# Kernel tuning notes

Measured on AMD Instinct MI355X. Metric: run time of the kernel, lower is better.

The kernel has to match this reference:

```python
import jax, jax.numpy as jnp
import numpy as np

D_MODEL = 1024
N_HEADS = 16
D_HEAD = D_MODEL // N_HEADS
D_FF = 4096
B, T = 2, 2048


def setup_inputs() -> dict:
    key = jax.random.key(0)
    ks = jax.random.split(key, 7)
    s = lambda fan_in: 1.0 / np.sqrt(fan_in)
    return {
        "x": jax.random.normal(ks[0], (B, T, D_MODEL), dtype=jnp.float32),
        "ln1_g": jnp.ones((D_MODEL,), jnp.float32),
        "ln1_b": jnp.zeros((D_MODEL,), jnp.float32),
        "w_qkv": jax.random.normal(ks[1], (D_MODEL, 3 * D_MODEL), jnp.float32) * s(D_MODEL),
        "w_proj": jax.random.normal(ks[2], (D_MODEL, D_MODEL), jnp.float32) * s(D_MODEL),
        "ln2_g": jnp.ones((D_MODEL,), jnp.float32),
        "ln2_b": jnp.zeros((D_MODEL,), jnp.float32),
        "w_fc1": jax.random.normal(ks[3], (D_MODEL, D_FF), jnp.float32) * s(D_MODEL),
        "w_fc2": jax.random.normal(ks[4], (D_FF, D_MODEL), jnp.float32) * s(D_FF),
    }


def _layernorm(x, g, b, eps=1e-5):
    mu = jnp.mean(x, axis=-1, keepdims=True)
    var = jnp.var(x, axis=-1, keepdims=True)
    return (x - mu) * jax.lax.rsqrt(var + eps) * g + b


def _attn(x, w_qkv, w_proj):
    Bx, Tx, d = x.shape
    qkv = x @ w_qkv  # [B,T,3d]
    q, k, v = jnp.split(qkv, 3, axis=-1)
    split = lambda t: t.reshape(Bx, Tx, N_HEADS, D_HEAD).transpose(0, 2, 1, 3)
    q, k, v = split(q), split(k), split(v)
    scores = jnp.einsum("bhqd,bhkd->bhqk", q, k) / np.sqrt(D_HEAD).astype(np.float32)
    mask = jnp.tril(jnp.ones((Tx, Tx), dtype=bool))
    scores = jnp.where(mask, scores, -jnp.inf)
    attn = jax.nn.softmax(scores, axis=-1)
    out = jnp.einsum("bhqk,bhkd->bhqd", attn, v)
    out = out.transpose(0, 2, 1, 3).reshape(Bx, Tx, d)
    return out @ w_proj


def reference(x, ln1_g, ln1_b, w_qkv, w_proj, ln2_g, ln2_b, w_fc1, w_fc2):
    x = x + _attn(_layernorm(x, ln1_g, ln1_b), w_qkv, w_proj)
    h = jax.nn.gelu(_layernorm(x, ln2_g, ln2_b) @ w_fc1, approximate=False)
    return x + h @ w_fc2
```

## Files before the change

kernel.cpp:

```cpp
#include <hip/hip_runtime.h>
#include <math.h>

using short8 = __attribute__((ext_vector_type(8))) short;
using f32x4  = __attribute__((ext_vector_type(4))) float;
typedef unsigned short ushort;

__device__ inline ushort f2bf(float f) {
    union { float f; unsigned int i; } v; v.f = f;
    unsigned int x = v.i;
    return (ushort)((x + 0x7FFFu + ((x >> 16) & 1u)) >> 16);
}
__device__ inline void st_out(float* p, float v) { *p = v; }
__device__ inline void st_out(ushort* p, float v) { *p = f2bf(v); }

__device__ inline void gl_lds16(const ushort* g, ushort* l) {
    __builtin_amdgcn_global_load_lds((const __attribute__((address_space(1))) unsigned int*)g,
                                     (__attribute__((address_space(3))) unsigned int*)l, 16, 0, 0);
}
#define MFMA __builtin_amdgcn_mfma_f32_16x16x32_bf16

__global__ __launch_bounds__(256) void ln_kernel(const float* __restrict__ x,
                                                 const float* __restrict__ g,
                                                 const float* __restrict__ b,
                                                 ushort* __restrict__ y) {
    int row = blockIdx.x;
    const float* xr = x + (size_t)row * 1024;
    int t = threadIdx.x;
    float v[4];
    float s = 0.f, s2 = 0.f;
#pragma unroll
    for (int i = 0; i < 4; i++) {
        v[i] = xr[t + i * 256];
        s += v[i]; s2 += v[i] * v[i];
    }
#pragma unroll
    for (int off = 1; off < 64; off <<= 1) {
        s += __shfl_xor(s, off); s2 += __shfl_xor(s2, off);
    }
    __shared__ float ps[8];
    int w = t >> 6;
    if ((t & 63) == 0) { ps[w] = s; ps[4 + w] = s2; }
    __syncthreads();
    s  = ps[0] + ps[1] + ps[2] + ps[3];
    s2 = ps[4] + ps[5] + ps[6] + ps[7];
    float mu   = s * (1.0f / 1024.0f);
    float var  = s2 * (1.0f / 1024.0f) - mu * mu;
    float rinv = rsqrtf(var + 1e-5f);
    ushort* yr = y + (size_t)row * 1024;
#pragma unroll
    for (int i = 0; i < 4; i++) {
        int c = t + i * 256;
        yr[c] = f2bf((v[i] - mu) * rinv * g[c] + b[c]);
    }
}

__global__ __launch_bounds__(256) void wt_kernel(const float* __restrict__ s,
                                                 ushort* __restrict__ d, int K, int N) {
    __shared__ float tile[32][33];
    int n0 = blockIdx.x * 32, k0 = blockIdx.y * 32;
    int tx = threadIdx.x & 31, ty = threadIdx.x >> 5;
#pragma unroll
    for (int i = 0; i < 4; i++)
        tile[ty + i * 8][tx] = s[(size_t)(k0 + ty + i * 8) * N + n0 + tx];
    __syncthreads();
#pragma unroll
    for (int i = 0; i < 4; i++)
        d[(size_t)(n0 + ty + i * 8) * K + k0 + tx] = f2bf(tile[tx][ty + i * 8]);
}

template <int EPI, typename CT>
__global__ __launch_bounds__(256) void gemm_kernel(const ushort* __restrict__ A,
                                                   const ushort* __restrict__ Bt,
                                                   CT* __restrict__ C,
                                                   const float* __restrict__ R,
                                                   ushort* __restrict__ VT,
                                                   int M, int N, int K) {
    __shared__ alignas(16) ushort As[128 * 32];
    __shared__ alignas(16) ushort Bs[128 * 32];
    int t = threadIdx.x, lane = t & 63, w = t >> 6;
    int bm = blockIdx.y * 128, bn = blockIdx.x * 128;
    int wm = (w >> 1) * 64, wn = (w & 1) * 64;
    f32x4 acc[4][4] = {};
    int srow = lane >> 2;
    int schunk = (lane & 3) ^ ((lane >> 3) & 3);
    int rs = lane & 15, qd = lane >> 4;

    for (int k0 = 0; k0 < K; k0 += 32) {
        __syncthreads();
#pragma unroll
        for (int i = 0; i < 2; i++) {
            int idx = w * 2 + i;
            gl_lds16(A  + (size_t)(bm + idx * 16 + srow) * K + k0 + schunk * 8, &As[idx * 512]);
            gl_lds16(Bt + (size_t)(bn + idx * 16 + srow) * K + k0 + schunk * 8, &Bs[idx * 512]);
        }
        __syncthreads();
        short8 af[4], bf[4];
#pragma unroll
        for (int i = 0; i < 4; i++) {
            int ml = wm + i * 16 + rs;
            af[i] = *(const short8*)&As[ml * 32 + ((qd ^ ((ml >> 1) & 3)) * 8)];
            int nl = wn + i * 16 + rs;
            bf[i] = *(const short8*)&Bs[nl * 32 + ((qd ^ ((nl >> 1) & 3)) * 8)];
        }
#pragma unroll
        for (int mi = 0; mi < 4; mi++)
#pragma unroll
            for (int ni = 0; ni < 4; ni++)
                acc[mi][ni] = MFMA(af[mi], bf[ni], acc[mi][ni], 0, 0, 0);
    }
#pragma unroll
    for (int mi = 0; mi < 4; mi++)
#pragma unroll
        for (int ni = 0; ni < 4; ni++) {
            int row = bm + wm + mi * 16 + qd * 4;
            int col = bn + wn + ni * 16 + rs;
            if (EPI == 3) {
                if (col < 2048) {
#pragma unroll
                    for (int r = 0; r < 4; r++)
                        ((ushort*)C)[(size_t)(row + r) * 2048 + col] = f2bf(acc[mi][ni][r]);
                } else {
                    int rel = col - 2048, hh = rel >> 6, dd = rel & 63;
                    ushort tmp[4];
#pragma unroll
                    for (int r = 0; r < 4; r++) tmp[r] = f2bf(acc[mi][ni][r]);
                    size_t base = ((size_t)((row >> 11) * 16 + hh) * 64 + dd) * 2048 + (row & 2047);
                    *(uint2*)&VT[base] = *(uint2*)tmp;
                }
            } else {
#pragma unroll
                for (int r = 0; r < 4; r++) {
                    float v = acc[mi][ni][r];
                    size_t idx = (size_t)(row + r) * N + col;
                    if (EPI == 1) v += R[idx];
                    if (EPI == 2) v = 0.5f * v * (1.0f + erff(v * 0.70710678118f));
                    st_out(&C[idx], v);
                }
            }
        }
}

template <int EPI, typename CT>
__global__ __launch_bounds__(256) void gemm_n64_kernel(const ushort* __restrict__ A,
                                                       const ushort* __restrict__ Bt,
                                                       CT* __restrict__ C,
                                                       const float* __restrict__ R,
                                                       int M, int N, int K) {
    __shared__ alignas(16) ushort As[128 * 32];
    __shared__ alignas(16) ushort Bs[64 * 32];
    int t = threadIdx.x, lane = t & 63, w = t >> 6;
    int bm = blockIdx.y * 128, bn = blockIdx.x * 64;
    int wm = (w >> 1) * 64, wn = (w & 1) * 32;
    f32x4 acc[4][2] = {};
    int srow = lane >> 2;
    int schunk = (lane & 3) ^ ((lane >> 3) & 3);
    int rs = lane & 15, qd = lane >> 4;

    for (int k0 = 0; k0 < K; k0 += 32) {
        __syncthreads();
#pragma unroll
        for (int i = 0; i < 2; i++) {
            int idx = w * 2 + i;
            gl_lds16(A + (size_t)(bm + idx * 16 + srow) * K + k0 + schunk * 8, &As[idx * 512]);
        }
        gl_lds16(Bt + (size_t)(bn + w * 16 + srow) * K + k0 + schunk * 8, &Bs[w * 512]);
        __syncthreads();
        short8 af[4], bf[2];
#pragma unroll
        for (int i = 0; i < 4; i++) {
            int ml = wm + i * 16 + rs;
            af[i] = *(const short8*)&As[ml * 32 + ((qd ^ ((ml >> 1) & 3)) * 8)];
        }
#pragma unroll
        for (int j = 0; j < 2; j++) {
            int nl = wn + j * 16 + rs;
            bf[j] = *(const short8*)&Bs[nl * 32 + ((qd ^ ((nl >> 1) & 3)) * 8)];
        }
#pragma unroll
        for (int mi = 0; mi < 4; mi++)
#pragma unroll
            for (int ni = 0; ni < 2; ni++)
                acc[mi][ni] = MFMA(af[mi], bf[ni], acc[mi][ni], 0, 0, 0);
    }
#pragma unroll
    for (int mi = 0; mi < 4; mi++)
#pragma unroll
        for (int ni = 0; ni < 2; ni++) {
            int row = bm + wm + mi * 16 + qd * 4;
            int col = bn + wn + ni * 16 + rs;
#pragma unroll
            for (int r = 0; r < 4; r++) {
                float v = acc[mi][ni][r];
                size_t idx = (size_t)(row + r) * N + col;
                if (EPI == 1) v += R[idx];
                if (EPI == 2) v = 0.5f * v * (1.0f + erff(v * 0.70710678118f));
                st_out(&C[idx], v);
            }
        }
}

__global__ __launch_bounds__(256) void attn_kernel(const ushort* __restrict__ qk,
                                                   const ushort* __restrict__ vT,
                                                   ushort* __restrict__ outp) {
    __shared__ alignas(16) ushort Ks[128 * 64];
    __shared__ alignas(16) ushort VTs[64 * 128];
    __shared__ alignas(16) ushort Ps[4 * 16 * 136];
    int t = threadIdx.x, lane = t & 63, w = t >> 6;
    int q0 = (int)(gridDim.x - 1 - blockIdx.x) * 64;
    int bh = blockIdx.y, bb = bh >> 4, h = bh & 15;
    const ushort* qkb = qk + (size_t)bb * 2048 * 2048;
    const ushort* qptr = qkb + h * 64;
    const ushort* kptr = qkb + 1024 + h * 64;
    const ushort* vtb  = vT + (size_t)bh * 64 * 2048;
    int rs = lane & 15, qd = lane >> 4;
    int qrow = q0 + w * 16 + rs;
    short8 aq0 = *(const short8*)(qptr + (size_t)qrow * 2048 + qd * 8);
    short8 aq1 = *(const short8*)(qptr + (size_t)qrow * 2048 + 32 + qd * 8);
    f32x4 o_acc[4] = {};
    float l_part[4] = {0.f, 0.f, 0.f, 0.f};
    int myq = q0 + w * 16 + qd * 4;
    int nk = (q0 + 63) / 128 + 1;
    int krl = lane >> 3, kch = lane & 7;
    int vrl = lane >> 4, vch = lane & 15;

    for (int kt = 0; kt < nk; kt++) {
        int k0 = kt * 128;
        __syncthreads();
#pragma unroll
        for (int i = 0; i < 4; i++) {
            int kk = w * 32 + i * 8 + krl;
            gl_lds16(kptr + (size_t)(k0 + kk) * 2048 + ((kch ^ (kk & 7)) * 8), &Ks[(w * 32 + i * 8) * 64]);
            int dd = w * 16 + i * 4 + vrl;
            gl_lds16(vtb + (size_t)dd * 2048 + k0 + ((vch ^ (dd & 15)) * 8), &VTs[(w * 16 + i * 4) * 128]);
        }
        __syncthreads();
        f32x4 s[8];
#pragma unroll
        for (int c = 0; c < 8; c++) {
            int kk = c * 16 + rs;
            short8 kf0 = *(const short8*)&Ks[kk * 64 + ((qd ^ (kk & 7)) * 8)];
            short8 kf1 = *(const short8*)&Ks[kk * 64 + (((qd + 4) ^ (kk & 7)) * 8)];
            f32x4 z = {};
            z = MFMA(aq0, kf0, z, 0, 0, 0);
            z = MFMA(aq1, kf1, z, 0, 0, 0);
            s[c] = z;
        }
        bool lastt = (kt == nk - 1);
#pragma unroll
        for (int c = 0; c < 8; c++) {
            int kk = k0 + c * 16 + rs;
#pragma unroll
            for (int r = 0; r < 4; r++) {
                float p = __expf(s[c][r] * 0.125f);
                if (lastt && (kk > myq + r)) p = 0.f;
                s[c][r] = p;
                l_part[r] += p;
            }
        }
#pragma unroll
        for (int r = 0; r < 4; r++)
#pragma unroll
            for (int c = 0; c < 8; c++)
                Ps[(w * 16 + qd * 4 + r) * 136 + c * 16 + rs] = f2bf(s[c][r]);
        short8 ap[4];
#pragma unroll
        for (int kc = 0; kc < 4; kc++)
            ap[kc] = *(const short8*)&Ps[(w * 16 + rs) * 136 + kc * 32 + qd * 8];
#pragma unroll
        for (int dt = 0; dt < 4; dt++) {
            int dd = dt * 16 + rs;
#pragma unroll
            for (int kc = 0; kc < 4; kc++) {
                int g = kc * 4 + qd;
                short8 bv = *(const short8*)&VTs[dd * 128 + ((g ^ (dd & 15)) * 8)];
                o_acc[dt] = MFMA(ap[kc], bv, o_acc[dt], 0, 0, 0);
            }
        }
    }
#pragma unroll
    for (int r = 0; r < 4; r++)
#pragma unroll
        for (int off = 1; off < 16; off <<= 1)
            l_part[r] += __shfl_xor(l_part[r], off);
#pragma unroll
    for (int dt = 0; dt < 4; dt++)
#pragma unroll
        for (int r = 0; r < 4; r++)
            outp[(size_t)(bb * 2048 + myq + r) * 1024 + h * 64 + dt * 16 + rs] = f2bf(o_acc[dt][r] / l_part[r]);
}

extern "C" void kernel_launch(void* const* d_in, const int* in_sizes, int n_in,
                              void* d_out, int out_size, void* d_ws, size_t ws_size,
                              hipStream_t stream) {
    const float* x     = (const float*)d_in[0];
    const float* ln1g  = (const float*)d_in[1];
    const float* ln1b  = (const float*)d_in[2];
    const float* wqkv  = (const float*)d_in[3];
    const float* wproj = (const float*)d_in[4];
    const float* ln2g  = (const float*)d_in[5];
    const float* ln2b  = (const float*)d_in[6];
    const float* wfc1  = (const float*)d_in[7];
    const float* wfc2  = (const float*)d_in[8];
    float* out = (float*)d_out;
    char* ws = (char*)d_ws;
    const size_t MB = 1024 * 1024;

    ushort* wbufA = (ushort*)(ws);
    ushort* lnbuf = (ushort*)(ws + 8 * MB);
    ushort* qk    = (ushort*)(ws + 16 * MB);
    ushort* vT    = (ushort*)(ws + 32 * MB);
    const int Rr = 4096;

    ln_kernel<<<Rr, 256, 0, stream>>>(x, ln1g, ln1b, lnbuf);
    wt_kernel<<<dim3(3072 / 32, 1024 / 32), 256, 0, stream>>>(wqkv, wbufA, 1024, 3072);
    gemm_kernel<3, ushort><<<dim3(3072 / 128, Rr / 128), 256, 0, stream>>>(lnbuf, wbufA, qk, nullptr, vT, Rr, 3072, 1024);
    attn_kernel<<<dim3(2048 / 64, 32), 256, 0, stream>>>(qk, vT, lnbuf);
    wt_kernel<<<dim3(1024 / 32, 1024 / 32), 256, 0, stream>>>(wproj, wbufA, 1024, 1024);
    gemm_n64_kernel<1, float><<<dim3(1024 / 64, Rr / 128), 256, 0, stream>>>(lnbuf, wbufA, out, x, Rr, 1024, 1024);
    ln_kernel<<<Rr, 256, 0, stream>>>(out, ln2g, ln2b, lnbuf);
    wt_kernel<<<dim3(4096 / 32, 1024 / 32), 256, 0, stream>>>(wfc1, wbufA, 1024, 4096);

    if (ws_size >= 56 * MB) {
        ushort* hmid  = qk;
        ushort* wbufB = (ushort*)(ws + 48 * MB);
        wt_kernel<<<dim3(1024 / 32, 4096 / 32), 256, 0, stream>>>(wfc2, wbufB, 4096, 1024);
        gemm_kernel<2, ushort><<<dim3(4096 / 128, Rr / 128), 256, 0, stream>>>(lnbuf, wbufA, hmid, nullptr, nullptr, Rr, 4096, 1024);
        gemm_n64_kernel<1, float><<<dim3(1024 / 64, Rr / 128), 256, 0, stream>>>(hmid, wbufB, out, out, Rr, 1024, 4096);
    } else {
        ushort* hmid  = qk;
        ushort* wbufB = (ushort*)(ws + 32 * MB);
        wt_kernel<<<dim3(1024 / 32, 4096 / 32), 256, 0, stream>>>(wfc2, wbufB, 4096, 1024);
        for (int hf = 0; hf < 2; hf++) {
            const ushort* lnh = lnbuf + (size_t)hf * 2048 * 1024;
            float* outh = out + (size_t)hf * 2048 * 1024;
            gemm_kernel<2, ushort><<<dim3(4096 / 128, 2048 / 128), 256, 0, stream>>>(lnh, wbufA, hmid, nullptr, nullptr, 2048, 4096, 1024);
            gemm_n64_kernel<1, float><<<dim3(1024 / 64, 2048 / 128), 256, 0, stream>>>(hmid, wbufB, outh, outh, 2048, 1024, 4096);
        }
    }
}
```

Measured before the change: 431.0 us.

## Split-K the fc2 GEMM with atomic accumulation and widen K tile to 64

The N=64 GEMM now stages a K=64 slice per iteration with an 8-way XOR swizzle, which halves the number of barrier pairs per K. Its grid is reordered so the M dimension is blockIdx.x. The fc2 projection is split over K into two z-slices that atomically add into the output, which already holds the residual, so the 256-block launch becomes 512 blocks for better CU fill. The cost is float atomics traffic, and the summation order is no longer deterministic.

```diff
diff --git a/kernel.cpp b/kernel.cpp
--- a/kernel.cpp
+++ b/kernel.cpp
@@ -145,42 +145,51 @@
                                                        const ushort* __restrict__ Bt,
                                                        CT* __restrict__ C,
                                                        const float* __restrict__ R,
-                                                       int M, int N, int K) {
-    __shared__ alignas(16) ushort As[128 * 32];
-    __shared__ alignas(16) ushort Bs[64 * 32];
+                                                       int M, int N, int K, int Kh) {
+    __shared__ alignas(16) ushort As[128 * 64];
+    __shared__ alignas(16) ushort Bs[64 * 64];
     int t = threadIdx.x, lane = t & 63, w = t >> 6;
-    int bm = blockIdx.y * 128, bn = blockIdx.x * 64;
+    int bm = blockIdx.x * 128, bn = blockIdx.y * 64;
+    int kbeg = blockIdx.z * Kh;
     int wm = (w >> 1) * 64, wn = (w & 1) * 32;
     f32x4 acc[4][2] = {};
-    int srow = lane >> 2;
-    int schunk = (lane & 3) ^ ((lane >> 3) & 3);
+    int srow = lane >> 3;
+    int schunk = (lane & 7) ^ (lane >> 3);
     int rs = lane & 15, qd = lane >> 4;
 
-    for (int k0 = 0; k0 < K; k0 += 32) {
-        __syncthreads();
+    for (int k0 = kbeg; k0 < kbeg + Kh; k0 += 64) {
+        __syncthreads();
+#pragma unroll
+        for (int i = 0; i < 4; i++) {
+            int rr = w * 32 + i * 8;
+            gl_lds16(A + (size_t)(bm + rr + srow) * K + k0 + schunk * 8, &As[rr * 64]);
+        }
 #pragma unroll
         for (int i = 0; i < 2; i++) {
-            int idx = w * 2 + i;
-            gl_lds16(A + (size_t)(bm + idx * 16 + srow) * K + k0 + schunk * 8, &As[idx * 512]);
-        }
-        gl_lds16(Bt + (size_t)(bn + w * 16 + srow) * K + k0 + schunk * 8, &Bs[w * 512]);
-        __syncthreads();
-        short8 af[4], bf[2];
-#pragma unroll
-        for (int i = 0; i < 4; i++) {
-            int ml = wm + i * 16 + rs;
-            af[i] = *(const short8*)&As[ml * 32 + ((qd ^ ((ml >> 1) & 3)) * 8)];
-        }
-#pragma unroll
-        for (int j = 0; j < 2; j++) {
-            int nl = wn + j * 16 + rs;
-            bf[j] = *(const short8*)&Bs[nl * 32 + ((qd ^ ((nl >> 1) & 3)) * 8)];
-        }
-#pragma unroll
-        for (int mi = 0; mi < 4; mi++)
-#pragma unroll
-            for (int ni = 0; ni < 2; ni++)
-                acc[mi][ni] = MFMA(af[mi], bf[ni], acc[mi][ni], 0, 0, 0);
+            int rr = w * 16 + i * 8;
+            gl_lds16(Bt + (size_t)(bn + rr + srow) * K + k0 + schunk * 8, &Bs[rr * 64]);
+        }
+        __syncthreads();
+#pragma unroll
+        for (int half = 0; half < 2; half++) {
+            int cq = qd + half * 4;
+            short8 af[4], bfr[2];
+#pragma unroll
+            for (int i = 0; i < 4; i++) {
+                int ml = wm + i * 16 + rs;
+                af[i] = *(const short8*)&As[ml * 64 + ((cq ^ (ml & 7)) * 8)];
+            }
+#pragma unroll
+            for (int j = 0; j < 2; j++) {
+                int nl = wn + j * 16 + rs;
+                bfr[j] = *(const short8*)&Bs[nl * 64 + ((cq ^ (nl & 7)) * 8)];
+            }
+#pragma unroll
+            for (int mi = 0; mi < 4; mi++)
+#pragma unroll
+                for (int ni = 0; ni < 2; ni++)
+                    acc[mi][ni] = MFMA(af[mi], bfr[ni], acc[mi][ni], 0, 0, 0);
+        }
     }
 #pragma unroll
     for (int mi = 0; mi < 4; mi++)
@@ -192,9 +201,12 @@
             for (int r = 0; r < 4; r++) {
                 float v = acc[mi][ni][r];
                 size_t idx = (size_t)(row + r) * N + col;
-                if (EPI == 1) v += R[idx];
-                if (EPI == 2) v = 0.5f * v * (1.0f + erff(v * 0.70710678118f));
-                st_out(&C[idx], v);
+                if (EPI == 4) {
+                    atomicAdd((float*)&C[idx], v);
+                } else {
+                    if (EPI == 1) v += R[idx];
+                    st_out(&C[idx], v);
+                }
             }
         }
 }
@@ -316,7 +328,7 @@
     gemm_kernel<3, ushort><<<dim3(3072 / 128, Rr / 128), 256, 0, stream>>>(lnbuf, wbufA, qk, nullptr, vT, Rr, 3072, 1024);
     attn_kernel<<<dim3(2048 / 64, 32), 256, 0, stream>>>(qk, vT, lnbuf);
     wt_kernel<<<dim3(1024 / 32, 1024 / 32), 256, 0, stream>>>(wproj, wbufA, 1024, 1024);
-    gemm_n64_kernel<1, float><<<dim3(1024 / 64, Rr / 128), 256, 0, stream>>>(lnbuf, wbufA, out, x, Rr, 1024, 1024);
+    gemm_n64_kernel<1, float><<<dim3(Rr / 128, 1024 / 64, 1), 256, 0, stream>>>(lnbuf, wbufA, out, x, Rr, 1024, 1024, 1024);
     ln_kernel<<<Rr, 256, 0, stream>>>(out, ln2g, ln2b, lnbuf);
     wt_kernel<<<dim3(4096 / 32, 1024 / 32), 256, 0, stream>>>(wfc1, wbufA, 1024, 4096);
 
@@ -325,7 +337,7 @@
         ushort* wbufB = (ushort*)(ws + 48 * MB);
         wt_kernel<<<dim3(1024 / 32, 4096 / 32), 256, 0, stream>>>(wfc2, wbufB, 4096, 1024);
         gemm_kernel<2, ushort><<<dim3(4096 / 128, Rr / 128), 256, 0, stream>>>(lnbuf, wbufA, hmid, nullptr, nullptr, Rr, 4096, 1024);
-        gemm_n64_kernel<1, float><<<dim3(1024 / 64, Rr / 128), 256, 0, stream>>>(hmid, wbufB, out, out, Rr, 1024, 4096);
+        gemm_n64_kernel<4, float><<<dim3(Rr / 128, 1024 / 64, 2), 256, 0, stream>>>(hmid, wbufB, out, nullptr, Rr, 1024, 4096, 2048);
     } else {
         ushort* hmid  = qk;
         ushort* wbufB = (ushort*)(ws + 32 * MB);
@@ -334,7 +346,7 @@
             const ushort* lnh = lnbuf + (size_t)hf * 2048 * 1024;
             float* outh = out + (size_t)hf * 2048 * 1024;
             gemm_kernel<2, ushort><<<dim3(4096 / 128, 2048 / 128), 256, 0, stream>>>(lnh, wbufA, hmid, nullptr, nullptr, 2048, 4096, 1024);
-            gemm_n64_kernel<1, float><<<dim3(1024 / 64, 2048 / 128), 256, 0, stream>>>(hmid, wbufB, outh, outh, 2048, 1024, 4096);
-        }
-    }
-}
+            gemm_n64_kernel<4, float><<<dim3(2048 / 128, 1024 / 64, 2), 256, 0, stream>>>(hmid, wbufB, outh, nullptr, 2048, 1024, 4096, 2048);
+        }
+    }
+}
```

After: 397.3 us. 1.08x faster.
